# Performance work log

Hardware: AMD Instinct MI355X
Metric: run time of the kernel (lower is better)

## Reference

```python
import jax, jax.numpy as jnp
import numpy as np

N = 50000       # nodes
E = 800000      # edges (avg degree 16)
F_IN = 20
HID = 500
OUT = 2
BN_EPS = 1e-5


def setup_inputs() -> dict:
    key = jax.random.key(0)
    k1, k2, k3, k4 = jax.random.split(key, 4)
    node_feature = jax.random.normal(k1, (N, F_IN), dtype=jnp.float32)
    edge_index = jax.random.randint(k2, (2, E), 0, N, dtype=jnp.int32)
    gcn_W = jax.random.normal(k3, (F_IN, HID), dtype=jnp.float32) * (1.0 / np.sqrt(F_IN))
    gcn_b = jnp.zeros((HID,), dtype=jnp.float32)
    bn_gamma = jnp.ones((HID,), dtype=jnp.float32)
    bn_beta = jnp.zeros((HID,), dtype=jnp.float32)
    lin_W = jax.random.normal(k4, (HID, OUT), dtype=jnp.float32) * (1.0 / np.sqrt(HID))
    lin_b = jnp.zeros((OUT,), dtype=jnp.float32)
    return {
        "node_feature": node_feature,
        "edge_index": edge_index,
        "gcn_W": gcn_W,
        "gcn_b": gcn_b,
        "bn_gamma": bn_gamma,
        "bn_beta": bn_beta,
        "lin_W": lin_W,
        "lin_b": lin_b,
    }


def reference(node_feature, edge_index, gcn_W, gcn_b, bn_gamma, bn_beta, lin_W, lin_b):
    n = node_feature.shape[0]
    # --- GCNConv: add self-loops, symmetric normalization, gather-scale-scatter ---
    loop = jnp.arange(n, dtype=edge_index.dtype)
    row = jnp.concatenate([edge_index[0], loop])   # sources
    col = jnp.concatenate([edge_index[1], loop])   # targets
    deg = jax.ops.segment_sum(jnp.ones(col.shape, jnp.float32), col, num_segments=n)
    dinv = jnp.where(deg > 0, jax.lax.rsqrt(jnp.maximum(deg, 1.0)), 0.0)
    norm = dinv[row] * dinv[col]                   # [E+N]
    h = node_feature @ gcn_W                       # [N, HID]
    msg = h[row] * norm[:, None]                   # [E+N, HID]
    agg = jax.ops.segment_sum(msg, col, num_segments=n) + gcn_b  # [N, HID]
    # --- BatchNorm1d (training mode: batch statistics, biased variance) ---
    mean = agg.mean(axis=0)
    var = agg.var(axis=0)
    xn = (agg - mean) * jax.lax.rsqrt(var + BN_EPS) * bn_gamma + bn_beta
    rsu_embedding = xn[0:1]                        # [1, HID]
    # --- Linear -> ReLU -> Softmax(dim=1) ---
    logits = jax.nn.relu(xn @ lin_W + lin_b)       # [N, OUT]
    action_prob = jax.nn.softmax(logits, axis=1)
    return action_prob, rsu_embedding
```

## Files before the change

kernel.cpp:

```cpp
#include <hip/hip_runtime.h>

#define F_IN 20
#define HID 500
#define N_STATS 420
#define BN_EPS 1e-5f
#define CAP 64
#define NXCD 8
#define XGROUPS 256
#define GNODES 64
#define GBT 320

__global__ void init_kernel(int* cnt, int n) {
    int i = blockIdx.x * blockDim.x + threadIdx.x;
    if (i < n) cnt[i] = 0;
}

__global__ void xfill_kernel(const int* __restrict__ ei, int* __restrict__ cnt,
                             unsigned short* __restrict__ srow, int E, int n) {
    int b = blockIdx.x;
    int g = b >> 3;
    int x = b & 7;
    int part = (n + NXCD - 1) / NXCD;
    int clo = x * part;
    int chi = clo + part; if (chi > n) chi = n;
    int cs = (((E + XGROUPS - 1) / XGROUPS) + 3) & ~3;
    int s = g * cs;
    if (s >= E) return;
    int e_end = s + cs; if (e_end > E) e_end = E;
    const int4* c4p = (const int4*)(ei + E);
    for (int q = (s >> 2) + threadIdx.x; (q << 2) < e_end; q += blockDim.x) {
        int4 c4 = c4p[q];
        int cc[4] = {c4.x, c4.y, c4.z, c4.w};
#pragma unroll
        for (int k = 0; k < 4; ++k) {
            int rel = cc[k] - clo;
            if ((unsigned)rel < (unsigned)(chi - clo)) {
                int r = ei[(q << 2) + k];
                int p = atomicAdd(&cnt[clo + rel], 1);
                if (p < CAP) srow[(size_t)(clo + rel) * CAP + p] = (unsigned short)r;
            }
        }
    }
}

__global__ void prescale_kernel(const float* __restrict__ x, const int* __restrict__ cnt,
                                float* __restrict__ y, float* __restrict__ dinv, int n) {
    int g = blockIdx.x * blockDim.x + threadIdx.x;
    int i = g / 5, c = g % 5;
    if (i >= n) return;
    float di = rsqrtf((float)(cnt[i] + 1));
    if (c == 0) dinv[i] = di;
    float4 v = *(const float4*)(x + (size_t)i * F_IN + 4 * c);
    v.x *= di; v.y *= di; v.z *= di; v.w *= di;
    *(float4*)(y + (size_t)i * F_IN + 4 * c) = v;
}

__global__ __launch_bounds__(GBT) void gather_stats_kernel(
    const float* __restrict__ y, const unsigned short* __restrict__ srow,
    const int* __restrict__ cnt, const float* __restrict__ dinv,
    float* __restrict__ aggx, float* __restrict__ partial, int n) {
    __shared__ float buf[GNODES * F_IN];
    int il = threadIdx.x / 5, c = threadIdx.x % 5;
    int i = blockIdx.x * GNODES + il;
    float4 acc = make_float4(0.f, 0.f, 0.f, 0.f);
    if (i < n) {
        float di = dinv[i];
        int mi = cnt[i];
        if (mi > CAP) mi = CAP;
        acc = *(const float4*)(y + (size_t)i * F_IN + 4 * c);
        const unsigned short* sp = srow + (size_t)i * CAP;
        int j = 0;
        for (; j + 16 <= mi; j += 16) {
            uint4 pa = *(const uint4*)(sp + j);
            uint4 pb = *(const uint4*)(sp + j + 8);
            int rr[16];
            rr[0] = pa.x & 0xffff; rr[1] = pa.x >> 16;
            rr[2] = pa.y & 0xffff; rr[3] = pa.y >> 16;
            rr[4] = pa.z & 0xffff; rr[5] = pa.z >> 16;
            rr[6] = pa.w & 0xffff; rr[7] = pa.w >> 16;
            rr[8]  = pb.x & 0xffff; rr[9]  = pb.x >> 16;
            rr[10] = pb.y & 0xffff; rr[11] = pb.y >> 16;
            rr[12] = pb.z & 0xffff; rr[13] = pb.z >> 16;
            rr[14] = pb.w & 0xffff; rr[15] = pb.w >> 16;
#pragma unroll
            for (int k = 0; k < 16; ++k) {
                float4 v = *(const float4*)(y + (size_t)rr[k] * F_IN + 4 * c);
                acc.x += v.x; acc.y += v.y; acc.z += v.z; acc.w += v.w;
            }
        }
        for (; j + 8 <= mi; j += 8) {
            uint4 pk = *(const uint4*)(sp + j);
            int rr[8];
            rr[0] = pk.x & 0xffff; rr[1] = pk.x >> 16;
            rr[2] = pk.y & 0xffff; rr[3] = pk.y >> 16;
            rr[4] = pk.z & 0xffff; rr[5] = pk.z >> 16;
            rr[6] = pk.w & 0xffff; rr[7] = pk.w >> 16;
#pragma unroll
            for (int k = 0; k < 8; ++k) {
                float4 v = *(const float4*)(y + (size_t)rr[k] * F_IN + 4 * c);
                acc.x += v.x; acc.y += v.y; acc.z += v.z; acc.w += v.w;
            }
        }
        for (; j < mi; ++j) {
            int r = sp[j];
            float4 v = *(const float4*)(y + (size_t)r * F_IN + 4 * c);
            acc.x += v.x; acc.y += v.y; acc.z += v.z; acc.w += v.w;
        }
        acc.x *= di; acc.y *= di; acc.z *= di; acc.w *= di;
        *(float4*)(aggx + (size_t)i * F_IN + 4 * c) = acc;
    }
    *(float4*)(buf + il * F_IN + 4 * c) = acc;
    __syncthreads();
    float s0 = 0.f, s1 = 0.f;
    int t = threadIdx.x;
    {
        int f1 = t / F_IN, f2 = t % F_IN;
        for (int r = 0; r < GNODES; ++r)
            s0 = fmaf(buf[r * F_IN + f1], buf[r * F_IN + f2], s0);
    }
    int u1 = t + GBT;
    if (u1 < N_STATS) {
        if (u1 < 400) {
            int f1 = u1 / F_IN, f2 = u1 % F_IN;
            for (int r = 0; r < GNODES; ++r)
                s1 = fmaf(buf[r * F_IN + f1], buf[r * F_IN + f2], s1);
        } else {
            int f = u1 - 400;
            for (int r = 0; r < GNODES; ++r) s1 += buf[r * F_IN + f];
        }
    }
    partial[(size_t)blockIdx.x * N_STATS + t] = s0;
    if (u1 < N_STATS) partial[(size_t)blockIdx.x * N_STATS + u1] = s1;
}

__global__ __launch_bounds__(256) void reduce420_kernel(const float* __restrict__ partial,
                                                        float* __restrict__ stats, int nblocks) {
    __shared__ float sh[256];
    int t = blockIdx.x;
    int tid = threadIdx.x;
    float acc = 0.f;
    for (int k = tid; k < nblocks; k += 256)
        acc += partial[(size_t)k * N_STATS + t];
    sh[tid] = acc;
    __syncthreads();
    for (int off = 128; off > 0; off >>= 1) {
        if (tid < off) sh[tid] += sh[tid + off];
        __syncthreads();
    }
    if (tid == 0) stats[t] = sh[0];
}

__global__ __launch_bounds__(512) void finalize_kernel(
    const float* __restrict__ aggx, const float* __restrict__ W, const float* __restrict__ b,
    const float* __restrict__ gamma, const float* __restrict__ beta,
    const float* __restrict__ linW, const float* __restrict__ linb,
    const float* __restrict__ stats, float* __restrict__ weff, float* __restrict__ out, int n) {
    __shared__ float mu[F_IN], M[400], a0[F_IN], sA[HID], tA[HID];
    int t = threadIdx.x;
    float inv_n = 1.0f / (float)n;
    if (t < 400) M[t] = stats[t] * inv_n;
    else if (t < N_STATS) mu[t - 400] = stats[t] * inv_n;
    if (t < F_IN) a0[t] = aggx[t];
    __syncthreads();
    if (t < HID) {
        float wv[F_IN];
#pragma unroll
        for (int f = 0; f < F_IN; ++f) wv[f] = W[f * HID + t];
        float mdot = 0.0f;
#pragma unroll
        for (int f = 0; f < F_IN; ++f) mdot = fmaf(mu[f], wv[f], mdot);
        float bj = b[t];
        float m = mdot + bj;
        float e2 = 0.0f;
        for (int f1 = 0; f1 < F_IN; ++f1) {
            float inner = 0.0f;
#pragma unroll
            for (int f2 = 0; f2 < F_IN; ++f2) inner = fmaf(M[f1 * F_IN + f2], wv[f2], inner);
            e2 = fmaf(wv[f1], inner, e2);
        }
        float ex2 = e2 + 2.0f * bj * mdot + bj * bj;
        float var = ex2 - m * m;
        float s = gamma[t] * rsqrtf(var + BN_EPS);
        float tt = beta[t] - m * s;
        sA[t] = s;
        tA[t] = tt;
        float dotv = 0.0f;
#pragma unroll
        for (int f = 0; f < F_IN; ++f) dotv = fmaf(a0[f], wv[f], dotv);
        out[2 * n + t] = (dotv + bj) * s + tt;
    }
    __syncthreads();
    if (t < 40) {
        int f = t >> 1, c = t & 1;
        float acc = 0.0f;
        for (int j = 0; j < HID; ++j)
            acc = fmaf(sA[j] * W[f * HID + j], linW[j * 2 + c], acc);
        weff[t] = acc;
    } else if (t < 42) {
        int c = t - 40;
        float acc = linb[c];
        for (int j = 0; j < HID; ++j)
            acc = fmaf(fmaf(b[j], sA[j], tA[j]), linW[j * 2 + c], acc);
        weff[40 + c] = acc;
    }
}

__global__ void output_kernel(const float* __restrict__ aggx, const float* __restrict__ weff,
                              float* __restrict__ out, int n) {
    __shared__ float wl[42];
    if (threadIdx.x < 42) wl[threadIdx.x] = weff[threadIdx.x];
    __syncthreads();
    int i = blockIdx.x * blockDim.x + threadIdx.x;
    if (i >= n) return;
    const float4* ap = (const float4*)(aggx + (size_t)i * F_IN);
    float l0 = wl[40], l1 = wl[41];
#pragma unroll
    for (int k = 0; k < 5; ++k) {
        float4 v = ap[k];
        l0 = fmaf(v.x, wl[2 * (4 * k + 0)], l0);
        l1 = fmaf(v.x, wl[2 * (4 * k + 0) + 1], l1);
        l0 = fmaf(v.y, wl[2 * (4 * k + 1)], l0);
        l1 = fmaf(v.y, wl[2 * (4 * k + 1) + 1], l1);
        l0 = fmaf(v.z, wl[2 * (4 * k + 2)], l0);
        l1 = fmaf(v.z, wl[2 * (4 * k + 2) + 1], l1);
        l0 = fmaf(v.w, wl[2 * (4 * k + 3)], l0);
        l1 = fmaf(v.w, wl[2 * (4 * k + 3) + 1], l1);
    }
    l0 = fmaxf(l0, 0.0f);
    l1 = fmaxf(l1, 0.0f);
    float mx = fmaxf(l0, l1);
    float e0 = expf(l0 - mx), e1 = expf(l1 - mx);
    float inv = 1.0f / (e0 + e1);
    float2 p = make_float2(e0 * inv, e1 * inv);
    *(float2*)(out + 2 * (size_t)i) = p;
}

extern "C" void kernel_launch(void* const* d_in, const int* in_sizes, int n_in,
                              void* d_out, int out_size, void* d_ws, size_t ws_size,
                              hipStream_t stream) {
    const float* x     = (const float*)d_in[0];
    const int*   ei    = (const int*)d_in[1];
    const float* W     = (const float*)d_in[2];
    const float* b     = (const float*)d_in[3];
    const float* gamma = (const float*)d_in[4];
    const float* beta  = (const float*)d_in[5];
    const float* linW  = (const float*)d_in[6];
    const float* linb  = (const float*)d_in[7];
    float* out = (float*)d_out;

    int n = in_sizes[0] / F_IN;
    int E = in_sizes[1] / 2;
    const int BT = 256;
    int gblocks = (n + GNODES - 1) / GNODES;

    int*   cnt     = (int*)d_ws;
    float* dinv    = (float*)(cnt + n);
    float* y       = dinv + n;
    float* aggx    = y + (size_t)F_IN * n;
    float* partial = aggx + (size_t)F_IN * n;
    float* stats   = partial + (size_t)gblocks * N_STATS;
    float* weff    = stats + N_STATS;
    unsigned short* srow = (unsigned short*)(weff + 64);

    hipLaunchKernelGGL(init_kernel, dim3((n + BT - 1) / BT), dim3(BT), 0, stream, cnt, n);
    hipLaunchKernelGGL(xfill_kernel, dim3(XGROUPS * NXCD), dim3(BT), 0, stream, ei, cnt, srow, E, n);
    hipLaunchKernelGGL(prescale_kernel, dim3((5 * n + BT - 1) / BT), dim3(BT), 0, stream, x, cnt, y, dinv, n);
    hipLaunchKernelGGL(gather_stats_kernel, dim3(gblocks), dim3(GBT), 0, stream,
                       y, srow, cnt, dinv, aggx, partial, n);
    hipLaunchKernelGGL(reduce420_kernel, dim3(N_STATS), dim3(256), 0, stream, partial, stats, gblocks);
    hipLaunchKernelGGL(finalize_kernel, dim3(1), dim3(512), 0, stream,
                       aggx, W, b, gamma, beta, linW, linb, stats, weff, out, n);
    hipLaunchKernelGGL(output_kernel, dim3((n + BT - 1) / BT), dim3(BT), 0, stream, aggx, weff, out, n);
}
```

Measured before the change: 168.8 us.

## Bin nodes by in-degree and gather in degree-sorted order

Adds a degree histogram, built in the prescale kernel, and a new binscatter kernel that builds a permutation grouping nodes by clamped in-degree. The gather kernel then processes nodes in that permuted order so the lanes of a wavefront have similar neighbor counts and diverge less. The 16-wide unrolled gather loop is also removed, leaving the 8-wide loop. In exchange it adds a kernel launch, heavily contended atomics on a few bin counters, and a perm indirection that breaks the contiguous node order for per-node loads and stores.

```diff
diff --git a/kernel.cpp b/kernel.cpp
--- a/kernel.cpp
+++ b/kernel.cpp
@@ -1,18 +1,21 @@
 #include <hip/hip_runtime.h>
+#include <stdint.h>
 
 #define F_IN 20
 #define HID 500
 #define N_STATS 420
 #define BN_EPS 1e-5f
 #define CAP 64
+#define NBINS 65
 #define NXCD 8
 #define XGROUPS 256
 #define GNODES 64
 #define GBT 320
 
-__global__ void init_kernel(int* cnt, int n) {
+__global__ void init_kernel(int* cnt, int* bcnt, int* bcur, int n) {
     int i = blockIdx.x * blockDim.x + threadIdx.x;
     if (i < n) cnt[i] = 0;
+    if (i < NBINS) { bcnt[i] = 0; bcur[i] = 0; }
 }
 
 __global__ void xfill_kernel(const int* __restrict__ ei, int* __restrict__ cnt,
@@ -44,50 +47,52 @@
 }
 
 __global__ void prescale_kernel(const float* __restrict__ x, const int* __restrict__ cnt,
-                                float* __restrict__ y, float* __restrict__ dinv, int n) {
+                                float* __restrict__ y, float* __restrict__ dinv,
+                                int* __restrict__ bcnt, int n) {
     int g = blockIdx.x * blockDim.x + threadIdx.x;
     int i = g / 5, c = g % 5;
     if (i >= n) return;
-    float di = rsqrtf((float)(cnt[i] + 1));
-    if (c == 0) dinv[i] = di;
+    int ci = cnt[i];
+    float di = rsqrtf((float)(ci + 1));
+    if (c == 0) {
+        dinv[i] = di;
+        int d = ci > CAP ? CAP : ci;
+        atomicAdd(&bcnt[d], 1);
+    }
     float4 v = *(const float4*)(x + (size_t)i * F_IN + 4 * c);
     v.x *= di; v.y *= di; v.z *= di; v.w *= di;
     *(float4*)(y + (size_t)i * F_IN + 4 * c) = v;
 }
 
+__global__ void binscatter_kernel(const int* __restrict__ cnt, const int* __restrict__ bcnt,
+                                  int* __restrict__ bcur, int* __restrict__ perm, int n) {
+    int i = blockIdx.x * blockDim.x + threadIdx.x;
+    if (i >= n) return;
+    int ci = cnt[i];
+    int d = ci > CAP ? CAP : ci;
+    int bstart = 0;
+    for (int k = 0; k < d; ++k) bstart += bcnt[k];
+    int pos = bstart + atomicAdd(&bcur[d], 1);
+    perm[pos] = i;
+}
+
 __global__ __launch_bounds__(GBT) void gather_stats_kernel(
     const float* __restrict__ y, const unsigned short* __restrict__ srow,
     const int* __restrict__ cnt, const float* __restrict__ dinv,
+    const int* __restrict__ perm,
     float* __restrict__ aggx, float* __restrict__ partial, int n) {
     __shared__ float buf[GNODES * F_IN];
     int il = threadIdx.x / 5, c = threadIdx.x % 5;
-    int i = blockIdx.x * GNODES + il;
+    int slot = blockIdx.x * GNODES + il;
     float4 acc = make_float4(0.f, 0.f, 0.f, 0.f);
-    if (i < n) {
+    if (slot < n) {
+        int i = perm[slot];
         float di = dinv[i];
         int mi = cnt[i];
         if (mi > CAP) mi = CAP;
         acc = *(const float4*)(y + (size_t)i * F_IN + 4 * c);
         const unsigned short* sp = srow + (size_t)i * CAP;
         int j = 0;
-        for (; j + 16 <= mi; j += 16) {
-            uint4 pa = *(const uint4*)(sp + j);
-            uint4 pb = *(const uint4*)(sp + j + 8);
-            int rr[16];
-            rr[0] = pa.x & 0xffff; rr[1] = pa.x >> 16;
-            rr[2] = pa.y & 0xffff; rr[3] = pa.y >> 16;
-            rr[4] = pa.z & 0xffff; rr[5] = pa.z >> 16;
-            rr[6] = pa.w & 0xffff; rr[7] = pa.w >> 16;
-            rr[8]  = pb.x & 0xffff; rr[9]  = pb.x >> 16;
-            rr[10] = pb.y & 0xffff; rr[11] = pb.y >> 16;
-            rr[12] = pb.z & 0xffff; rr[13] = pb.z >> 16;
-            rr[14] = pb.w & 0xffff; rr[15] = pb.w >> 16;
-#pragma unroll
-            for (int k = 0; k < 16; ++k) {
-                float4 v = *(const float4*)(y + (size_t)rr[k] * F_IN + 4 * c);
-                acc.x += v.x; acc.y += v.y; acc.z += v.z; acc.w += v.w;
-            }
-        }
         for (; j + 8 <= mi; j += 8) {
             uint4 pk = *(const uint4*)(sp + j);
             int rr[8];
@@ -260,13 +265,19 @@
     float* partial = aggx + (size_t)F_IN * n;
     float* stats   = partial + (size_t)gblocks * N_STATS;
     float* weff    = stats + N_STATS;
-    unsigned short* srow = (unsigned short*)(weff + 64);
-
-    hipLaunchKernelGGL(init_kernel, dim3((n + BT - 1) / BT), dim3(BT), 0, stream, cnt, n);
+    int*   perm    = (int*)(weff + 64);
+    int*   bcnt    = perm + n;
+    int*   bcur    = bcnt + NBINS;
+    unsigned short* srow = (unsigned short*)(((uintptr_t)(bcur + NBINS) + 15) & ~(uintptr_t)15);
+
+    hipLaunchKernelGGL(init_kernel, dim3((n + BT - 1) / BT), dim3(BT), 0, stream, cnt, bcnt, bcur, n);
     hipLaunchKernelGGL(xfill_kernel, dim3(XGROUPS * NXCD), dim3(BT), 0, stream, ei, cnt, srow, E, n);
-    hipLaunchKernelGGL(prescale_kernel, dim3((5 * n + BT - 1) / BT), dim3(BT), 0, stream, x, cnt, y, dinv, n);
+    hipLaunchKernelGGL(prescale_kernel, dim3((5 * n + BT - 1) / BT), dim3(BT), 0, stream,
+                       x, cnt, y, dinv, bcnt, n);
+    hipLaunchKernelGGL(binscatter_kernel, dim3((n + BT - 1) / BT), dim3(BT), 0, stream,
+                       cnt, bcnt, bcur, perm, n);
     hipLaunchKernelGGL(gather_stats_kernel, dim3(gblocks), dim3(GBT), 0, stream,
-                       y, srow, cnt, dinv, aggx, partial, n);
+                       y, srow, cnt, dinv, perm, aggx, partial, n);
     hipLaunchKernelGGL(reduce420_kernel, dim3(N_STATS), dim3(256), 0, stream, partial, stats, gblocks);
     hipLaunchKernelGGL(finalize_kernel, dim3(1), dim3(512), 0, stream,
                        aggx, W, b, gamma, beta, linW, linb, stats, weff, out, n);
```

After: 457.6 us. +171.1%, slower.
